# Kernel tuning notes

Hardware: AMD Instinct MI355X
Metric: run time of the kernel (lower is better)

The kernel has to match this reference:

```python
import jax, jax.numpy as jnp
import numpy as np

B, S, D, H = 4, 2048, 1024, 16
HD = D // H
NEG = -1000000.0  # matches sequence_mask fill value in the torch source


def setup_inputs() -> dict:
    key = jax.random.key(0)
    kq, kk, kv, kl, k1, k2, k3, k4 = jax.random.split(key, 8)
    scale = 1.0 / np.sqrt(D)
    return {
        "queries": jax.random.normal(kq, (B, S, D), dtype=jnp.float32),
        "keys": jax.random.normal(kk, (B, S, D), dtype=jnp.float32),
        "values": jax.random.normal(kv, (B, S, D), dtype=jnp.float32),
        "valid_lens": jax.random.randint(kl, (B,), 0, S, dtype=jnp.int64),
        "Wq": jax.random.normal(k1, (D, D), dtype=jnp.float32) * scale,
        "Wk": jax.random.normal(k2, (D, D), dtype=jnp.float32) * scale,
        "Wv": jax.random.normal(k3, (D, D), dtype=jnp.float32) * scale,
        "Wo": jax.random.normal(k4, (D, D), dtype=jnp.float32) * scale,
    }


def reference(queries, keys, values, valid_lens, Wq, Wk, Wv, Wo):
    def split_heads(x):  # [B,S,D] -> [B,H,S,HD]
        return x.reshape(B, S, H, HD).transpose(0, 2, 1, 3)

    q = split_heads(queries @ Wq)
    k = split_heads(keys @ Wk)
    v = split_heads(values @ Wv)

    scores = jnp.einsum("bhqd,bhkd->bhqk", q, k) / np.sqrt(HD)
    # padding mask over key positions: key index < valid_len[b]
    key_mask = jnp.arange(S)[None, :] < valid_lens[:, None]  # [B,S]
    scores = jnp.where(key_mask[:, None, None, :], scores, NEG)
    attn = jax.nn.softmax(scores, axis=-1)
    # dropout p=0.0 -> identity
    out = jnp.einsum("bhqk,bhkd->bhqd", attn, v)
    out = out.transpose(0, 2, 1, 3).reshape(B, S, D)  # merge heads
    return out @ Wo
```

## Files before the change

kernel.cpp:

```cpp
#include <hip/hip_runtime.h>
#include <hip/hip_bf16.h>

#define B_ 4
#define S_ 2048
#define D_ 1024
#define H_ 16
#define HD_ 64
#define M_ 8192
#define NEGV -1000000.0f
#define CEXP 0.18033688011112042f

typedef __attribute__((ext_vector_type(8))) __bf16 bf16x8;
typedef __attribute__((ext_vector_type(4))) float f32x4;
typedef __attribute__((ext_vector_type(16))) float f32x16;

__device__ __forceinline__ f32x4 mfma16(bf16x8 a, bf16x8 b, f32x4 c) {
  return __builtin_amdgcn_mfma_f32_16x16x32_bf16(a, b, c, 0, 0, 0);
}
__device__ __forceinline__ f32x16 mfma32(bf16x8 a, bf16x8 b, f32x16 c) {
  return __builtin_amdgcn_mfma_f32_32x32x16_bf16(a, b, c, 0, 0, 0);
}

#if __has_builtin(__builtin_amdgcn_exp2f)
__device__ __forceinline__ float exp2_hw(float x) { return __builtin_amdgcn_exp2f(x); }
#else
__device__ __forceinline__ float exp2_hw(float x) {
  float r;
  asm volatile("v_exp_f32 %0, %1" : "=v"(r) : "v"(x));
  return r;
}
#endif

__device__ __forceinline__ unsigned bf16rz(float x) {
  unsigned u = __float_as_uint(x);
  return (u + 0x7FFFu + ((u >> 16) & 1u)) >> 16;
}
__device__ __forceinline__ unsigned pk2bf(float a, float b) {
  unsigned ua = __float_as_uint(a), ub = __float_as_uint(b);
  ua = ua + 0x7FFFu + ((ua >> 16) & 1u);
  ub = ub + 0x7FFFu + ((ub >> 16) & 1u);
  return (ua >> 16) | (ub & 0xFFFF0000u);
}

__device__ __forceinline__ void gld_lds16(const __hip_bfloat16* g, __hip_bfloat16* l) {
  __builtin_amdgcn_global_load_lds(
      (const __attribute__((address_space(1))) void*)g,
      (__attribute__((address_space(3))) void*)l, 16, 0, 0);
}

__global__ __launch_bounds__(256) void convert_x3(const float* __restrict__ Xq,
                                                  const float* __restrict__ Xk,
                                                  const float* __restrict__ Xv,
                                                  __hip_bfloat16* __restrict__ Yq,
                                                  __hip_bfloat16* __restrict__ Yk,
                                                  __hip_bfloat16* __restrict__ Yv,
                                                  int n4, const int* __restrict__ vl) {
  const int z = blockIdx.y;
  const float* X = (z == 0) ? Xq : (z == 1) ? Xk : Xv;
  __hip_bfloat16* Y = (z == 0) ? Yq : (z == 1) ? Yk : Yv;
  int i = blockIdx.x * blockDim.x + threadIdx.x;
  if (i >= n4) return;
  if (z) {
    int gm = i >> 8;
    int vlen = vl[gm >> 11];
    if (vlen > 0 && (gm & 2047) >= ((vlen + 63) & ~63)) return;
  }
  float4 v = reinterpret_cast<const float4*>(X)[i];
  uint2 o;
  o.x = pk2bf(v.x, v.y);
  o.y = pk2bf(v.z, v.w);
  reinterpret_cast<uint2*>(Y)[i] = o;
}

__global__ __launch_bounds__(256) void convert_wt4(const float* __restrict__ W0,
                                                   const float* __restrict__ W1,
                                                   const float* __restrict__ W2,
                                                   const float* __restrict__ W3,
                                                   __hip_bfloat16* __restrict__ WtBase) {
  const int z = blockIdx.z;
  const float* W = (z == 0) ? W0 : (z == 1) ? W1 : (z == 2) ? W2 : W3;
  __hip_bfloat16* Wt = WtBase + (size_t)z * D_ * D_;
  __shared__ float tile[32][33];
  int c0 = blockIdx.x * 32, r0 = blockIdx.y * 32;
  int tx = threadIdx.x, ty = threadIdx.y;
#pragma unroll
  for (int rr = ty; rr < 32; rr += 8)
    tile[rr][tx] = W[(size_t)(r0 + rr) * D_ + c0 + tx];
  __syncthreads();
#pragma unroll
  for (int rr = ty; rr < 32; rr += 8)
    reinterpret_cast<unsigned short*>(Wt)[(size_t)(c0 + rr) * D_ + r0 + tx] =
        (unsigned short)bf16rz(tile[tx][rr]);
}

__global__ __launch_bounds__(256) void gemm_qkv(const __hip_bfloat16* __restrict__ Aq,
                                                const __hip_bfloat16* __restrict__ Ak,
                                                const __hip_bfloat16* __restrict__ Av,
                                                const __hip_bfloat16* __restrict__ WtBase,
                                                __hip_bfloat16* __restrict__ Qh,
                                                __hip_bfloat16* __restrict__ Kh,
                                                __hip_bfloat16* __restrict__ Vh,
                                                const int* __restrict__ vl) {
  const int z = blockIdx.z;
  const __hip_bfloat16* A = (z == 0) ? Aq : (z == 1) ? Ak : Av;
  const __hip_bfloat16* Bt = WtBase + (size_t)z * D_ * D_;
  __hip_bfloat16* Cout = (z == 0) ? Qh : (z == 1) ? Kh : Vh;
  const float cscale = (z == 0) ? CEXP : 1.0f;
  const int epi = (z == 2) ? 1 : 0;

  int id = blockIdx.y * gridDim.x + blockIdx.x;
  int cpx = (gridDim.x * gridDim.y) >> 3;
  int nid = (id & 7) * cpx + (id >> 3);
  const int m0 = (nid >> 3) * 128, n0 = (nid & 7) * 128;
  if (z) {
    int vlen = vl[m0 >> 11];
    if (vlen > 0 && (m0 & 2047) >= ((vlen + 63) & ~63)) return;
  }
  const int t = threadIdx.x, lane = t & 63, wid = t >> 6;
  const int lc = lane & 15, g = lane >> 4;
  const int srow8 = lane >> 3, sg8 = lane & 7;
  __shared__ __align__(16) __hip_bfloat16 smem[2][2][128 * 64];
  f32x4 acc[4][4] = {};
  const int wm = (wid & 1) * 64, wn = (wid >> 1) * 64;

  auto stage = [&](int buf, int k0) {
#pragma unroll
    for (int c = 0; c < 4; ++c) {
      int ci = c * 4 + wid;
      int row = ci * 8 + srow8;
      int sg = sg8 ^ (row & 7);
      gld_lds16(A + (size_t)(m0 + row) * D_ + k0 + sg * 8, &smem[buf][0][ci * 512]);
      gld_lds16(Bt + (size_t)(n0 + row) * D_ + k0 + sg * 8, &smem[buf][1][ci * 512]);
    }
  };

  stage(0, 0);
  asm volatile("s_waitcnt vmcnt(0)" ::: "memory");
  __syncthreads();
  int cur = 0;

  for (int kt = 0; kt < D_ / 64; ++kt) {
    if (kt + 1 < D_ / 64) stage(cur ^ 1, (kt + 1) * 64);
    const __hip_bfloat16* As = smem[cur][0];
    const __hip_bfloat16* Bs = smem[cur][1];
#pragma unroll
    for (int kh = 0; kh < 2; ++kh) {
      bf16x8 af[4], bf[4];
#pragma unroll
      for (int mi = 0; mi < 4; ++mi) {
        int r = wm + mi * 16 + lc;
        af[mi] = *reinterpret_cast<const bf16x8*>(
            As + r * 64 + (((kh * 4 + g) ^ (r & 7)) << 3));
        int rn = wn + mi * 16 + lc;
        bf[mi] = *reinterpret_cast<const bf16x8*>(
            Bs + rn * 64 + (((kh * 4 + g) ^ (rn & 7)) << 3));
      }
#pragma unroll
      for (int mi = 0; mi < 4; ++mi)
#pragma unroll
        for (int ni = 0; ni < 4; ++ni)
          acc[mi][ni] = mfma16(af[mi], bf[ni], acc[mi][ni]);
    }
    asm volatile("s_waitcnt vmcnt(0)" ::: "memory");
    __syncthreads();
    cur ^= 1;
  }

#pragma unroll
  for (int mi = 0; mi < 4; ++mi) {
#pragma unroll
    for (int ni = 0; ni < 4; ++ni) {
#pragma unroll
      for (int i = 0; i < 4; ++i) {
        int gm = m0 + wm + mi * 16 + g * 4 + i;
        int gn = n0 + wn + ni * 16 + lc;
        float val = acc[mi][ni][i] * cscale;
        int b = gm >> 11, s = gm & 2047, h = gn >> 6, d = gn & 63;
        if (epi == 0) {
          reinterpret_cast<unsigned short*>(
              Cout)[(((size_t)(b * H_ + h) * S_ + s) << 6) + d] =
              (unsigned short)bf16rz(val);
        } else {
          reinterpret_cast<unsigned short*>(
              Cout)[(((size_t)(b * H_ + h) * HD_ + d) << 11) + s] =
              (unsigned short)bf16rz(val);
        }
      }
    }
  }
}

template <int EPI>
__global__ __launch_bounds__(256) void gemm_bt(const __hip_bfloat16* __restrict__ A,
                                               const __hip_bfloat16* __restrict__ Bt,
                                               void* __restrict__ Cout,
                                               const int* __restrict__ vskip,
                                               float cscale) {
  int id = blockIdx.y * gridDim.x + blockIdx.x;
  int cpx = (gridDim.x * gridDim.y) >> 3;
  int nid = (id & 7) * cpx + (id >> 3);
  const int m0 = (nid >> 3) * 128, n0 = (nid & 7) * 128;
  if (vskip) {
    int vlen = vskip[m0 >> 11];
    if (vlen > 0 && (m0 & 2047) >= ((vlen + 63) & ~63)) return;
  }
  const int t = threadIdx.x, lane = t & 63, wid = t >> 6;
  const int lc = lane & 15, g = lane >> 4;
  const int srow8 = lane >> 3, sg8 = lane & 7;
  __shared__ __align__(16) __hip_bfloat16 smem[2][2][128 * 64];
  f32x4 acc[4][4] = {};
  const int wm = (wid & 1) * 64, wn = (wid >> 1) * 64;

  auto stage = [&](int buf, int k0) {
#pragma unroll
    for (int c = 0; c < 4; ++c) {
      int ci = c * 4 + wid;
      int row = ci * 8 + srow8;
      int sg = sg8 ^ (row & 7);
      gld_lds16(A + (size_t)(m0 + row) * D_ + k0 + sg * 8, &smem[buf][0][ci * 512]);
      gld_lds16(Bt + (size_t)(n0 + row) * D_ + k0 + sg * 8, &smem[buf][1][ci * 512]);
    }
  };

  stage(0, 0);
  asm volatile("s_waitcnt vmcnt(0)" ::: "memory");
  __syncthreads();
  int cur = 0;

  for (int kt = 0; kt < D_ / 64; ++kt) {
    if (kt + 1 < D_ / 64) stage(cur ^ 1, (kt + 1) * 64);
    const __hip_bfloat16* As = smem[cur][0];
    const __hip_bfloat16* Bs = smem[cur][1];
#pragma unroll
    for (int kh = 0; kh < 2; ++kh) {
      bf16x8 af[4], bf[4];
#pragma unroll
      for (int mi = 0; mi < 4; ++mi) {
        int r = wm + mi * 16 + lc;
        af[mi] = *reinterpret_cast<const bf16x8*>(
            As + r * 64 + (((kh * 4 + g) ^ (r & 7)) << 3));
        int rn = wn + mi * 16 + lc;
        bf[mi] = *reinterpret_cast<const bf16x8*>(
            Bs + rn * 64 + (((kh * 4 + g) ^ (rn & 7)) << 3));
      }
#pragma unroll
      for (int mi = 0; mi < 4; ++mi)
#pragma unroll
        for (int ni = 0; ni < 4; ++ni)
          acc[mi][ni] = mfma16(af[mi], bf[ni], acc[mi][ni]);
    }
    asm volatile("s_waitcnt vmcnt(0)" ::: "memory");
    __syncthreads();
    cur ^= 1;
  }

#pragma unroll
  for (int mi = 0; mi < 4; ++mi) {
#pragma unroll
    for (int ni = 0; ni < 4; ++ni) {
#pragma unroll
      for (int i = 0; i < 4; ++i) {
        int gm = m0 + wm + mi * 16 + g * 4 + i;
        int gn = n0 + wn + ni * 16 + lc;
        float val = acc[mi][ni][i] * cscale;
        if constexpr (EPI == 0) {
          int b = gm >> 11, s = gm & 2047, h = gn >> 6, d = gn & 63;
          reinterpret_cast<unsigned short*>(
              Cout)[(((size_t)(b * H_ + h) * S_ + s) << 6) + d] =
              (unsigned short)bf16rz(val);
        } else if constexpr (EPI == 1) {
          int b = gm >> 11, s = gm & 2047, h = gn >> 6, d = gn & 63;
          reinterpret_cast<unsigned short*>(
              Cout)[(((size_t)(b * H_ + h) * HD_ + d) << 11) + s] =
              (unsigned short)bf16rz(val);
        } else {
          ((float*)Cout)[(size_t)gm * D_ + gn] = val;
        }
      }
    }
  }
}

__global__ __launch_bounds__(512) void attn(const __hip_bfloat16* __restrict__ Qh,
                                            const __hip_bfloat16* __restrict__ Kh,
                                            const __hip_bfloat16* __restrict__ Vt,
                                            const int* __restrict__ vlens,
                                            __hip_bfloat16* __restrict__ O,
                                            int* __restrict__ ctr) {
  const int t = threadIdx.x, lane = t & 63, w = t >> 6;
  const int wq = w & 3, up = w >> 2;
  const int q = lane & 31;
  const int hh = lane >> 5;

  int va = vlens[0], vb = vlens[1], vc = vlens[2], vd = vlens[3];
  int ia = 0, ib = 1, ic = 2, id_ = 3;
  {
    int tv, ti;
#define CSWAP(x, xi, y, yi) \
    if (y > x) { tv = x; x = y; y = tv; ti = xi; xi = yi; yi = ti; }
    CSWAP(va, ia, vb, ib) CSWAP(vc, ic, vd, id_)
    CSWAP(va, ia, vc, ic) CSWAP(vb, ib, vd, id_)
    CSWAP(vb, ib, vc, ic)
#undef CSWAP
  }
  __shared__ int s_unit;
  __shared__ __align__(16) __hip_bfloat16 smem[3][8192];

  while (true) {
    if (t == 0) s_unit = atomicAdd(ctr, 1);
    __syncthreads();
    const int u = s_unit;
    if (u >= 512) break;
    const int rank = u >> 7;
    const int b = (rank == 0) ? ia : (rank == 1) ? ib : (rank == 2) ? ic : id_;
    const int vlen = (rank == 0) ? va : (rank == 1) ? vb : (rank == 2) ? vc : vd;
    const int r = u & 127;
    const int h = r & 15, qtp = r >> 4;
    const int bh = b * 16 + h;

    const __hip_bfloat16* Qb = Qh + (size_t)bh * S_ * HD_;
    const __hip_bfloat16* Kb = Kh + (size_t)bh * S_ * HD_;
    const __hip_bfloat16* Vb = Vt + (size_t)bh * HD_ * S_;

    const int qrow = qtp * 256 + up * 128 + wq * 32 + q;
    bf16x8 qf[4];
#pragma unroll
    for (int kk = 0; kk < 4; ++kk)
      qf[kk] = *reinterpret_cast<const bf16x8*>(Qb + (size_t)qrow * HD_ + kk * 16 + hh * 8);

    f32x16 accT[2] = {};
    float l_half = 0.f;

    const int srow = lane >> 3;
    const int sg = lane & 7;
    const float maskv = (vlen == 0) ? 0.f : NEGV;
    const int kv_end = (vlen == 0) ? S_ : min(S_, (vlen + 63) & ~63);
    const int nt = kv_end >> 6;

    auto stage = [&](int buf, int tile) {
      int kv = tile * 64;
      int rr = w * 8 + srow;
      int gs = sg ^ (rr & 7);
      gld_lds16(Kb + (size_t)(kv + rr) * HD_ + gs * 8, smem[buf] + (w * 8) * 64);
      gld_lds16(Vb + (size_t)rr * S_ + kv + gs * 8, smem[buf] + 4096 + (w * 8) * 64);
    };

    stage(0, 0);
    if (nt > 1) stage(1, 1);
    int bc = 0;
    int bs = (nt > 2) ? 2 : 0;

    for (int tt = 0; tt < nt; ++tt) {
      if (tt + 1 < nt) {
        asm volatile("s_waitcnt vmcnt(2)" ::: "memory");
      } else {
        asm volatile("s_waitcnt vmcnt(0)" ::: "memory");
      }
      __syncthreads();
      if (tt + 2 < nt) stage(bs, tt + 2);

      const __hip_bfloat16* Ks = smem[bc];
      const __hip_bfloat16* Vs = smem[bc] + 4096;

      f32x16 sc[2];
      __builtin_amdgcn_s_setprio(1);
#pragma unroll
      for (int ct = 0; ct < 2; ++ct) {
        f32x16 a = {};
#pragma unroll
        for (int kk = 0; kk < 4; ++kk) {
          int row = ct * 32 + q;
          bf16x8 kf = *reinterpret_cast<const bf16x8*>(
              Ks + row * 64 + (((kk * 2 + hh) ^ (row & 7)) << 3));
          a = mfma32(kf, qf[kk], a);
        }
        sc[ct] = a;
      }
      __builtin_amdgcn_s_setprio(0);

      int kv = tt * 64;
      if (kv + 64 > vlen) {
#pragma unroll
        for (int ct = 0; ct < 2; ++ct)
#pragma unroll
          for (int rr = 0; rr < 16; ++rr) {
            int j = kv + ct * 32 + (rr & 3) + 8 * (rr >> 2) + 4 * hh;
            if (j >= vlen) sc[ct][rr] = maskv;
          }
      }

      uint wlo[8], whi[8];
      float rs = 0.f;
#pragma unroll
      for (int a2 = 0; a2 < 8; ++a2) {
        float p0 = exp2_hw(sc[a2 >> 2][(a2 & 3) * 4 + 0]);
        float p1 = exp2_hw(sc[a2 >> 2][(a2 & 3) * 4 + 1]);
        float p2 = exp2_hw(sc[a2 >> 2][(a2 & 3) * 4 + 2]);
        float p3 = exp2_hw(sc[a2 >> 2][(a2 & 3) * 4 + 3]);
        rs += (p0 + p1) + (p2 + p3);
        wlo[a2] = pk2bf(p0, p1);
        whi[a2] = pk2bf(p2, p3);
      }
      l_half += rs;

      __builtin_amdgcn_s_setprio(1);
#pragma unroll
      for (int kk = 0; kk < 4; ++kk) {
        uint glo = wlo[2 * kk], ghi = whi[2 * kk];
        uint flo = wlo[2 * kk + 1], fhi = whi[2 * kk + 1];
        uint slo = hh ? glo : flo, shi = hh ? ghi : fhi;
        uint rlo = __shfl_xor(slo, 32), rhi = __shfl_xor(shi, 32);
        union { uint u[4]; bf16x8 v; } pf;
        pf.u[0] = hh ? rlo : glo;
        pf.u[1] = hh ? rhi : ghi;
        pf.u[2] = hh ? flo : rlo;
        pf.u[3] = hh ? fhi : rhi;
#pragma unroll
        for (int ctd = 0; ctd < 2; ++ctd) {
          int vr = ctd * 32 + q;
          bf16x8 vf = *reinterpret_cast<const bf16x8*>(
              Vs + vr * 64 + (((kk * 2 + hh) ^ (vr & 7)) << 3));
          accT[ctd] = mfma32(vf, pf.v, accT[ctd]);
        }
      }
      __builtin_amdgcn_s_setprio(0);
      bc = (bc == 2) ? 0 : bc + 1;
      bs = (bs == 2) ? 0 : bs + 1;
    }
    __syncthreads();

    float l_tot = l_half + __shfl_xor(l_half, 32);
    float inv = 1.f / l_tot;
    __hip_bfloat16* Ot = smem[0] + w * 2048;
#pragma unroll
    for (int ctd = 0; ctd < 2; ++ctd)
#pragma unroll
      for (int a2 = 0; a2 < 4; ++a2) {
        uint2 o;
        o.x = pk2bf(accT[ctd][a2 * 4 + 0] * inv, accT[ctd][a2 * 4 + 1] * inv);
        o.y = pk2bf(accT[ctd][a2 * 4 + 2] * inv, accT[ctd][a2 * 4 + 3] * inv);
        int gs8 = (ctd * 8 + a2 * 2 + hh) ^ ((q & 7) << 1);
        *reinterpret_cast<uint2*>(Ot + q * 64 + gs8 * 4) = o;
      }
#pragma unroll
    for (int rr = 0; rr < 4; ++rr) {
      int row = rr * 8 + (lane >> 3);
      int c16 = lane & 7;
      float4 v4 = *reinterpret_cast<const float4*>(
          Ot + row * 64 + (((c16 * 2) ^ ((row & 7) << 1)) << 2));
      int s = qtp * 256 + up * 128 + wq * 32 + row;
      *reinterpret_cast<float4*>(O + ((size_t)b * S_ + s) * D_ + h * HD_ + c16 * 8) = v4;
    }
  }
}

extern "C" void kernel_launch(void* const* d_in, const int* in_sizes, int n_in,
                              void* d_out, int out_size, void* d_ws, size_t ws_size,
                              hipStream_t stream) {
  const float* Xq = (const float*)d_in[0];
  const float* Xk = (const float*)d_in[1];
  const float* Xv = (const float*)d_in[2];
  const int* vl = (const int*)d_in[3];
  const float* Wq = (const float*)d_in[4];
  const float* Wk = (const float*)d_in[5];
  const float* Wv = (const float*)d_in[6];
  const float* Wo = (const float*)d_in[7];
  float* out = (float*)d_out;

  char* ws = (char*)d_ws;
  const size_t XB = (size_t)M_ * D_ * 2;
  const size_t WB = (size_t)D_ * D_ * 2;
  __hip_bfloat16* xq = (__hip_bfloat16*)(ws);
  __hip_bfloat16* xk = (__hip_bfloat16*)(ws + XB);
  __hip_bfloat16* xv = (__hip_bfloat16*)(ws + 2 * XB);
  __hip_bfloat16* wtq = (__hip_bfloat16*)(ws + 3 * XB);
  __hip_bfloat16* wto = (__hip_bfloat16*)(ws + 3 * XB + 3 * WB);
  __hip_bfloat16* Qh = (__hip_bfloat16*)(ws + 3 * XB + 4 * WB);
  __hip_bfloat16* Kh = (__hip_bfloat16*)(ws + 4 * XB + 4 * WB);
  __hip_bfloat16* Vh = (__hip_bfloat16*)(ws + 5 * XB + 4 * WB);
  __hip_bfloat16* Obuf = xq;
  int* ctr = (int*)xk;

  convert_wt4<<<dim3(32, 32, 4), dim3(32, 8), 0, stream>>>(Wq, Wk, Wv, Wo, wtq);

  const int n4 = M_ * D_ / 4;
  convert_x3<<<dim3(n4 / 256, 3), 256, 0, stream>>>(Xq, Xk, Xv, xq, xk, xv, n4, vl);

  gemm_qkv<<<dim3(M_ / 128, D_ / 128, 3), 256, 0, stream>>>(xq, xk, xv, wtq,
                                                            Qh, Kh, Vh, vl);

  hipMemsetAsync(ctr, 0, sizeof(int), stream);
  attn<<<dim3(512), 512, 0, stream>>>(Qh, Kh, Vh, vl, Obuf, ctr);
  gemm_bt<2><<<dim3(M_ / 128, D_ / 128), 256, 0, stream>>>(Obuf, wto, out, nullptr, 1.0f);
}
```

Before: 205.7 us.

## Split KV range across two wave groups per block and combine partial sums

```diff
diff --git a/kernel.cpp b/kernel.cpp
--- a/kernel.cpp
+++ b/kernel.cpp
@@ -288,7 +288,7 @@
                                             __hip_bfloat16* __restrict__ O,
                                             int* __restrict__ ctr) {
   const int t = threadIdx.x, lane = t & 63, w = t >> 6;
-  const int wq = w & 3, up = w >> 2;
+  const int gp = w >> 2, wq = w & 3;
   const int q = lane & 31;
   const int hh = lane >> 5;
 
@@ -304,25 +304,25 @@
 #undef CSWAP
   }
   __shared__ int s_unit;
-  __shared__ __align__(16) __hip_bfloat16 smem[3][8192];
+  __shared__ __align__(16) __hip_bfloat16 smem[2][2][8192];
 
   while (true) {
     if (t == 0) s_unit = atomicAdd(ctr, 1);
     __syncthreads();
     const int u = s_unit;
-    if (u >= 512) break;
-    const int rank = u >> 7;
+    if (u >= 1024) break;
+    const int rank = u >> 8;
     const int b = (rank == 0) ? ia : (rank == 1) ? ib : (rank == 2) ? ic : id_;
     const int vlen = (rank == 0) ? va : (rank == 1) ? vb : (rank == 2) ? vc : vd;
-    const int r = u & 127;
-    const int h = r & 15, qtp = r >> 4;
+    const int r = u & 255;
+    const int h = r & 15, qt = r >> 4;
     const int bh = b * 16 + h;
 
     const __hip_bfloat16* Qb = Qh + (size_t)bh * S_ * HD_;
     const __hip_bfloat16* Kb = Kh + (size_t)bh * S_ * HD_;
     const __hip_bfloat16* Vb = Vt + (size_t)bh * HD_ * S_;
 
-    const int qrow = qtp * 256 + up * 128 + wq * 32 + q;
+    const int qrow = qt * 128 + wq * 32 + q;
     bf16x8 qf[4];
 #pragma unroll
     for (int kk = 0; kk < 4; ++kk)
@@ -336,120 +336,148 @@
     const float maskv = (vlen == 0) ? 0.f : NEGV;
     const int kv_end = (vlen == 0) ? S_ : min(S_, (vlen + 63) & ~63);
     const int nt = kv_end >> 6;
-
-    auto stage = [&](int buf, int tile) {
-      int kv = tile * 64;
-      int rr = w * 8 + srow;
-      int gs = sg ^ (rr & 7);
-      gld_lds16(Kb + (size_t)(kv + rr) * HD_ + gs * 8, smem[buf] + (w * 8) * 64);
-      gld_lds16(Vb + (size_t)rr * S_ + kv + gs * 8, smem[buf] + 4096 + (w * 8) * 64);
+    const int nth = (nt + 1) >> 1;
+    const int g0 = gp ? nth : 0;
+    const int nloc = gp ? (nt - nth) : nth;
+
+    auto stage = [&](int buf, int tt) {
+      int kv = (g0 + tt) * 64;
+#pragma unroll
+      for (int c = 0; c < 2; ++c) {
+        int rr = wq * 16 + c * 8 + srow;
+        int gs = sg ^ (rr & 7);
+        gld_lds16(Kb + (size_t)(kv + rr) * HD_ + gs * 8,
+                  smem[gp][buf] + (wq * 16 + c * 8) * 64);
+        gld_lds16(Vb + (size_t)rr * S_ + kv + gs * 8,
+                  smem[gp][buf] + 4096 + (wq * 16 + c * 8) * 64);
+      }
     };
 
-    stage(0, 0);
-    if (nt > 1) stage(1, 1);
-    int bc = 0;
-    int bs = (nt > 2) ? 2 : 0;
-
-    for (int tt = 0; tt < nt; ++tt) {
-      if (tt + 1 < nt) {
-        asm volatile("s_waitcnt vmcnt(2)" ::: "memory");
-      } else {
-        asm volatile("s_waitcnt vmcnt(0)" ::: "memory");
-      }
+    if (nloc > 0) stage(0, 0);
+    asm volatile("s_waitcnt vmcnt(0)" ::: "memory");
+    __syncthreads();
+    int cur = 0;
+
+    for (int tt = 0; tt < nth; ++tt) {
+      const bool act = tt < nloc;
+      if (act && tt + 1 < nloc) stage(cur ^ 1, tt + 1);
+      if (act) {
+        const __hip_bfloat16* Ks = smem[gp][cur];
+        const __hip_bfloat16* Vs = smem[gp][cur] + 4096;
+
+        f32x16 sc[2];
+#pragma unroll
+        for (int ct = 0; ct < 2; ++ct) {
+          f32x16 a = {};
+#pragma unroll
+          for (int kk = 0; kk < 4; ++kk) {
+            int row = ct * 32 + q;
+            bf16x8 kf = *reinterpret_cast<const bf16x8*>(
+                Ks + row * 64 + (((kk * 2 + hh) ^ (row & 7)) << 3));
+            a = mfma32(kf, qf[kk], a);
+          }
+          sc[ct] = a;
+        }
+
+        int kv = (g0 + tt) * 64;
+        if (kv + 64 > vlen) {
+#pragma unroll
+          for (int ct = 0; ct < 2; ++ct)
+#pragma unroll
+            for (int rr = 0; rr < 16; ++rr) {
+              int j = kv + ct * 32 + (rr & 3) + 8 * (rr >> 2) + 4 * hh;
+              if (j >= vlen) sc[ct][rr] = maskv;
+            }
+        }
+
+        uint wlo[8], whi[8];
+        float rs = 0.f;
+#pragma unroll
+        for (int a2 = 0; a2 < 8; ++a2) {
+          float p0 = exp2_hw(sc[a2 >> 2][(a2 & 3) * 4 + 0]);
+          float p1 = exp2_hw(sc[a2 >> 2][(a2 & 3) * 4 + 1]);
+          float p2 = exp2_hw(sc[a2 >> 2][(a2 & 3) * 4 + 2]);
+          float p3 = exp2_hw(sc[a2 >> 2][(a2 & 3) * 4 + 3]);
+          rs += (p0 + p1) + (p2 + p3);
+          wlo[a2] = pk2bf(p0, p1);
+          whi[a2] = pk2bf(p2, p3);
+        }
+        l_half += rs;
+
+#pragma unroll
+        for (int kk = 0; kk < 4; ++kk) {
+          uint glo = wlo[2 * kk], ghi = whi[2 * kk];
+          uint flo = wlo[2 * kk + 1], fhi = whi[2 * kk + 1];
+          uint slo = hh ? glo : flo, shi = hh ? ghi : fhi;
+          uint rlo = __shfl_xor(slo, 32), rhi = __shfl_xor(shi, 32);
+          union { uint u[4]; bf16x8 v; } pf;
+          pf.u[0] = hh ? rlo : glo;
+          pf.u[1] = hh ? rhi : ghi;
+          pf.u[2] = hh ? flo : rlo;
+          pf.u[3] = hh ? fhi : rhi;
+#pragma unroll
+          for (int ctd = 0; ctd < 2; ++ctd) {
+            int vr = ctd * 32 + q;
+            bf16x8 vf = *reinterpret_cast<const bf16x8*>(
+                Vs + vr * 64 + (((kk * 2 + hh) ^ (vr & 7)) << 3));
+            accT[ctd] = mfma32(vf, pf.v, accT[ctd]);
+          }
+        }
+      }
+      asm volatile("s_waitcnt vmcnt(0)" ::: "memory");
       __syncthreads();
-      if (tt + 2 < nt) stage(bs, tt + 2);
-
-      const __hip_bfloat16* Ks = smem[bc];
-      const __hip_bfloat16* Vs = smem[bc] + 4096;
-
-      f32x16 sc[2];
-      __builtin_amdgcn_s_setprio(1);
-#pragma unroll
-      for (int ct = 0; ct < 2; ++ct) {
-        f32x16 a = {};
-#pragma unroll
-        for (int kk = 0; kk < 4; ++kk) {
-          int row = ct * 32 + q;
-          bf16x8 kf = *reinterpret_cast<const bf16x8*>(
-              Ks + row * 64 + (((kk * 2 + hh) ^ (row & 7)) << 3));
-          a = mfma32(kf, qf[kk], a);
-        }
-        sc[ct] = a;
-      }
-      __builtin_amdgcn_s_setprio(0);
-
-      int kv = tt * 64;
-      if (kv + 64 > vlen) {
-#pragma unroll
-        for (int ct = 0; ct < 2; ++ct)
-#pragma unroll
-          for (int rr = 0; rr < 16; ++rr) {
-            int j = kv + ct * 32 + (rr & 3) + 8 * (rr >> 2) + 4 * hh;
-            if (j >= vlen) sc[ct][rr] = maskv;
-          }
-      }
-
-      uint wlo[8], whi[8];
-      float rs = 0.f;
-#pragma unroll
-      for (int a2 = 0; a2 < 8; ++a2) {
-        float p0 = exp2_hw(sc[a2 >> 2][(a2 & 3) * 4 + 0]);
-        float p1 = exp2_hw(sc[a2 >> 2][(a2 & 3) * 4 + 1]);
-        float p2 = exp2_hw(sc[a2 >> 2][(a2 & 3) * 4 + 2]);
-        float p3 = exp2_hw(sc[a2 >> 2][(a2 & 3) * 4 + 3]);
-        rs += (p0 + p1) + (p2 + p3);
-        wlo[a2] = pk2bf(p0, p1);
-        whi[a2] = pk2bf(p2, p3);
-      }
-      l_half += rs;
-
-      __builtin_amdgcn_s_setprio(1);
-#pragma unroll
-      for (int kk = 0; kk < 4; ++kk) {
-        uint glo = wlo[2 * kk], ghi = whi[2 * kk];
-        uint flo = wlo[2 * kk + 1], fhi = whi[2 * kk + 1];
-        uint slo = hh ? glo : flo, shi = hh ? ghi : fhi;
-        uint rlo = __shfl_xor(slo, 32), rhi = __shfl_xor(shi, 32);
-        union { uint u[4]; bf16x8 v; } pf;
-        pf.u[0] = hh ? rlo : glo;
-        pf.u[1] = hh ? rhi : ghi;
-        pf.u[2] = hh ? flo : rlo;
-        pf.u[3] = hh ? fhi : rhi;
-#pragma unroll
-        for (int ctd = 0; ctd < 2; ++ctd) {
-          int vr = ctd * 32 + q;
-          bf16x8 vf = *reinterpret_cast<const bf16x8*>(
-              Vs + vr * 64 + (((kk * 2 + hh) ^ (vr & 7)) << 3));
-          accT[ctd] = mfma32(vf, pf.v, accT[ctd]);
-        }
-      }
-      __builtin_amdgcn_s_setprio(0);
-      bc = (bc == 2) ? 0 : bc + 1;
-      bs = (bs == 2) ? 0 : bs + 1;
+      cur ^= 1;
+    }
+
+    float* comb = (float*)smem;
+    float* combl = ((float*)smem) + 8192;
+    const int idx = wq * 64 + lane;
+    if (gp == 1) {
+#pragma unroll
+      for (int ctd = 0; ctd < 2; ++ctd)
+#pragma unroll
+        for (int a2 = 0; a2 < 4; ++a2)
+          *reinterpret_cast<float4*>(comb + idx * 32 + ctd * 16 + a2 * 4) =
+              make_float4(accT[ctd][a2 * 4 + 0], accT[ctd][a2 * 4 + 1],
+                          accT[ctd][a2 * 4 + 2], accT[ctd][a2 * 4 + 3]);
+      combl[idx] = l_half;
     }
     __syncthreads();
-
-    float l_tot = l_half + __shfl_xor(l_half, 32);
-    float inv = 1.f / l_tot;
-    __hip_bfloat16* Ot = smem[0] + w * 2048;
-#pragma unroll
-    for (int ctd = 0; ctd < 2; ++ctd)
-#pragma unroll
-      for (int a2 = 0; a2 < 4; ++a2) {
-        uint2 o;
-        o.x = pk2bf(accT[ctd][a2 * 4 + 0] * inv, accT[ctd][a2 * 4 + 1] * inv);
-        o.y = pk2bf(accT[ctd][a2 * 4 + 2] * inv, accT[ctd][a2 * 4 + 3] * inv);
-        int gs8 = (ctd * 8 + a2 * 2 + hh) ^ ((q & 7) << 1);
-        *reinterpret_cast<uint2*>(Ot + q * 64 + gs8 * 4) = o;
-      }
-#pragma unroll
-    for (int rr = 0; rr < 4; ++rr) {
-      int row = rr * 8 + (lane >> 3);
-      int c16 = lane & 7;
-      float4 v4 = *reinterpret_cast<const float4*>(
-          Ot + row * 64 + (((c16 * 2) ^ ((row & 7) << 1)) << 2));
-      int s = qtp * 256 + up * 128 + wq * 32 + row;
-      *reinterpret_cast<float4*>(O + ((size_t)b * S_ + s) * D_ + h * HD_ + c16 * 8) = v4;
+    if (gp == 0) {
+#pragma unroll
+      for (int ctd = 0; ctd < 2; ++ctd)
+#pragma unroll
+        for (int a2 = 0; a2 < 4; ++a2) {
+          float4 v4 = *reinterpret_cast<const float4*>(comb + idx * 32 + ctd * 16 + a2 * 4);
+          accT[ctd][a2 * 4 + 0] += v4.x;
+          accT[ctd][a2 * 4 + 1] += v4.y;
+          accT[ctd][a2 * 4 + 2] += v4.z;
+          accT[ctd][a2 * 4 + 3] += v4.w;
+        }
+      l_half += combl[idx];
+
+      float l_tot = l_half + __shfl_xor(l_half, 32);
+      float inv = 1.f / l_tot;
+      __hip_bfloat16* Ot = ((__hip_bfloat16*)smem) + 20480 + wq * 2048;
+#pragma unroll
+      for (int ctd = 0; ctd < 2; ++ctd)
+#pragma unroll
+        for (int a2 = 0; a2 < 4; ++a2) {
+          uint2 o;
+          o.x = pk2bf(accT[ctd][a2 * 4 + 0] * inv, accT[ctd][a2 * 4 + 1] * inv);
+          o.y = pk2bf(accT[ctd][a2 * 4 + 2] * inv, accT[ctd][a2 * 4 + 3] * inv);
+          int gs8 = (ctd * 8 + a2 * 2 + hh) ^ ((q & 7) << 1);
+          *reinterpret_cast<uint2*>(Ot + q * 64 + gs8 * 4) = o;
+        }
+#pragma unroll
+      for (int rr = 0; rr < 4; ++rr) {
+        int row = rr * 8 + (lane >> 3);
+        int c16 = lane & 7;
+        float4 v4 = *reinterpret_cast<const float4*>(
+            Ot + row * 64 + (((c16 * 2) ^ ((row & 7) << 1)) << 2));
+        int s = qt * 128 + wq * 32 + row;
+        *reinterpret_cast<float4*>(O + ((size_t)b * S_ + s) * D_ + h * HD_ + c16 * 8) = v4;
+      }
     }
   }
 }
```

Measured after the change: 210.3 us. 1.02x slower.
